# Optimization experiments

Measured on AMD Instinct MI355X. Metric: run time of the kernel, lower is better.

The kernel has to match this reference:

```python
import jax, jax.numpy as jnp
import numpy as np

NUM_HEADS = 16
PROJECT_DIM = 1024
HEAD_DIM = PROJECT_DIM // NUM_HEADS  # 64; used only for the softmax scale


def setup_inputs() -> dict:
    key = jax.random.key(0)
    k1, k2, k3 = jax.random.split(key, 3)
    B, N, D = 8, 3072, PROJECT_DIM
    inputs = jax.random.normal(k1, (B, N, D), dtype=jnp.float32)
    wqkv = jax.random.normal(k2, (D, 3 * D), dtype=jnp.float32) * (1.0 / np.sqrt(D))
    dense_w = jax.random.normal(k3, (3 * D, D), dtype=jnp.float32) * (1.0 / np.sqrt(3 * D))
    dense_b = jnp.zeros((D,), dtype=jnp.float32)
    return {"inputs": inputs, "wqkv": wqkv, "dense_w": dense_w, "dense_b": dense_b}


def reference(inputs, wqkv, dense_w, dense_b):
    B, N, D = inputs.shape
    H = NUM_HEADS
    # fused QKV projection: [B, N, 3D]
    qkv = jnp.einsum('bnd,de->bne', inputs, wqkv)
    # separate heads: [B, H, N, 3*head_dim]
    qkv = qkv.reshape(B, N, H, (3 * D) // H).transpose(0, 2, 1, 3)
    # NOTE: faithful to source — split along TOKEN axis (axis=2) into 3 chunks
    q, k, v = jnp.split(qkv, 3, axis=2)  # each [B, H, N//3, 3*head_dim]
    scale = 1.0 / jnp.sqrt(jnp.float32(HEAD_DIM))
    logits = jnp.einsum('bhqc,bhkc->bhqk', q, k) * scale  # [B, H, N//3, N//3]
    attn = jax.nn.softmax(logits, axis=-1)
    out = jnp.einsum('bhqk,bhkc->bhqc', attn, v)  # [B, H, N//3, 3*head_dim]
    # recombine heads -> [B, N//3, 3D]
    out = out.transpose(0, 2, 1, 3).reshape(B, N // 3, 3 * D)
    # output projection -> [B, N//3, D]
    return jnp.einsum('bnc,cd->bnd', out, dense_w) + dense_b
```

## Files before the change

### kernel.cpp

```cpp
#include <hip/hip_runtime.h>
#include <hip/hip_bf16.h>

typedef unsigned short u16;
using f32x4  = __attribute__((ext_vector_type(4))) float;
using bf16x8 = __attribute__((ext_vector_type(8))) short;

typedef __attribute__((address_space(1))) const void global_cvoid;
typedef __attribute__((address_space(3))) void lds_void;

__device__ __forceinline__ void async16(const u16* g, u16* l) {
    __builtin_amdgcn_global_load_lds((global_cvoid*)g, (lds_void*)l, 16, 0, 0);
}

__device__ __forceinline__ u16 f2bf(float f) {
    union { float f; unsigned u; } cv; cv.f = f;
    unsigned r = cv.u + 0x7fff + ((cv.u >> 16) & 1);
    return (u16)(r >> 16);
}

__device__ __forceinline__ u16 f2bf_rz(float f) {
    union { float f; unsigned u; } cv; cv.f = f;
    return (u16)(cv.u >> 16);
}

__device__ __forceinline__ float dppmax16(float x) {
    union { float f; int i; } c, o;
    c.f = x;
    o.i = __builtin_amdgcn_update_dpp(0, c.i, 0xB1,  0xF, 0xF, true); c.f = fmaxf(c.f, o.f);
    o.i = __builtin_amdgcn_update_dpp(0, c.i, 0x4E,  0xF, 0xF, true); c.f = fmaxf(c.f, o.f);
    o.i = __builtin_amdgcn_update_dpp(0, c.i, 0x141, 0xF, 0xF, true); c.f = fmaxf(c.f, o.f);
    o.i = __builtin_amdgcn_update_dpp(0, c.i, 0x140, 0xF, 0xF, true); c.f = fmaxf(c.f, o.f);
    return c.f;
}

__global__ __launch_bounds__(256) void cast_kernel(const float* __restrict__ src,
                                                   u16* __restrict__ dst, int n4) {
    int i = blockIdx.x * blockDim.x + threadIdx.x;
    int st = gridDim.x * blockDim.x;
    for (; i < n4; i += st) {
        float4 v = ((const float4*)src)[i];
        ushort4 o;
        o.x = f2bf(v.x); o.y = f2bf(v.y); o.z = f2bf(v.z); o.w = f2bf(v.w);
        ((ushort4*)dst)[i] = o;
    }
}

__global__ __launch_bounds__(256) void wtrans_kernel(const float* __restrict__ src,
                                                     u16* __restrict__ dst, int R, int C) {
    __shared__ float tile[64][68];
    int ct = blockIdx.x, rt = blockIdx.y;
    int t = threadIdx.x;
    int r = t >> 2;
    const float* s = src + (size_t)(rt * 64 + r) * C + ct * 64;
#pragma unroll
    for (int jj = 0; jj < 4; ++jj) {
        int c4 = (t & 3) + jj * 4;
        float4 v = *(const float4*)(s + c4 * 4);
        *(float4*)&tile[r][c4 * 4] = v;
    }
    __syncthreads();
    int od = t >> 2;
    u16* d = dst + (size_t)(ct * 64 + od) * R + rt * 64;
#pragma unroll
    for (int jj = 0; jj < 4; ++jj) {
        int c4 = (t & 3) + jj * 4;
        ushort4 v;
        v.x = f2bf(tile[c4 * 4 + 0][od]);
        v.y = f2bf(tile[c4 * 4 + 1][od]);
        v.z = f2bf(tile[c4 * 4 + 2][od]);
        v.w = f2bf(tile[c4 * 4 + 3][od]);
        *(ushort4*)(d + c4 * 4) = v;
    }
}

template<bool OUT_F32>
__global__ __launch_bounds__(256, 2)
void gemm_bt_kernel(const u16* __restrict__ A, const u16* __restrict__ BT,
                    void* __restrict__ Cout, const float* __restrict__ bias,
                    u16* __restrict__ VTout,
                    int M, int N, int K) {
    __shared__ u16 lA[128 * 64];
    __shared__ u16 lB[128 * 64];
    const int t = threadIdx.x;
    const int w = t >> 6, lane = t & 63;
    const int nbx = N >> 7;
    const int nwg = gridDim.x;
    int bid = blockIdx.x;
    int cpx = nwg >> 3;
    int swz = (bid & 7) * cpx + (bid >> 3);
    const int bx = swz % nbx;
    const int by = swz / nbx;
    const size_t m0 = (size_t)by * 128, n0 = (size_t)bx * 128;

    const int lr = lane >> 3;
    const int lc = (lane & 7) * 8;
    const int wr = (w >> 1) * 64, wc = (w & 1) * 64;

    f32x4 acc[4][4] = {};

    for (int kk = 0; kk < K; kk += 64) {
        __syncthreads();
#pragma unroll
        for (int i = 0; i < 4; ++i) {
            int rr = (w * 4 + i) * 8 + lr;
            async16(A  + (m0 + rr) * (size_t)K + kk + lc, &lA[(w * 4 + i) * 512]);
            async16(BT + (n0 + rr) * (size_t)K + kk + lc, &lB[(w * 4 + i) * 512]);
        }
        __syncthreads();
#pragma unroll
        for (int ks = 0; ks < 2; ++ks) {
            bf16x8 af[4], bfv[4];
#pragma unroll
            for (int m = 0; m < 4; ++m)
                af[m] = *(const bf16x8*)&lA[(wr + m * 16 + (lane & 15)) * 64 + ks * 32 + (lane >> 4) * 8];
#pragma unroll
            for (int n = 0; n < 4; ++n)
                bfv[n] = *(const bf16x8*)&lB[(wc + n * 16 + (lane & 15)) * 64 + ks * 32 + (lane >> 4) * 8];
#pragma unroll
            for (int m = 0; m < 4; ++m)
#pragma unroll
                for (int n = 0; n < 4; ++n)
                    acc[m][n] = __builtin_amdgcn_mfma_f32_16x16x32_bf16(af[m], bfv[n], acc[m][n], 0, 0, 0);
        }
    }

    const int r0 = (lane >> 4) * 4;
    const int cl = lane & 15;
    if constexpr (OUT_F32) {
        float* C = (float*)Cout;
#pragma unroll
        for (int m = 0; m < 4; ++m) {
            size_t row = m0 + wr + m * 16 + r0;
#pragma unroll
            for (int n = 0; n < 4; ++n) {
                size_t col = n0 + wc + n * 16 + cl;
                float bv = bias[col];
#pragma unroll
                for (int r = 0; r < 4; ++r)
                    C[(row + r) * (size_t)N + col] = acc[m][n][r] + bv;
            }
        }
    } else {
        u16* C = (u16*)Cout;
#pragma unroll
        for (int m = 0; m < 4; ++m) {
            size_t row = m0 + wr + m * 16 + r0;
#pragma unroll
            for (int n = 0; n < 4; ++n) {
                size_t col = n0 + wc + n * 16 + cl;
#pragma unroll
                for (int r = 0; r < 4; ++r)
                    C[(row + r) * (size_t)N + col] = f2bf(acc[m][n][r]);
            }
        }
    }
}

__global__ __launch_bounds__(512, 2)
void gemm256_kernel(const u16* __restrict__ A, const u16* __restrict__ BT,
                    u16* __restrict__ Cout, u16* __restrict__ VTout,
                    int M, int N, int K) {
    __shared__ u16 lds[65536];
    u16* lA = lds;
    u16* lB = lds + 32768;

    const int t = threadIdx.x, w = t >> 6, l = t & 63;
    const int g = l >> 4, ql = l & 15;
    const int wm = w >> 2, wn = w & 3;
    const int nbx = N >> 8;
    int bid = blockIdx.x;
    int cpx = gridDim.x >> 3;
    int swz = (bid & 7) * cpx + (bid >> 3);
    const int bx = swz % nbx, by = swz / nbx;
    const size_t m0 = (size_t)by * 256, n0 = (size_t)bx * 256;

    const u16* Ag = A  + m0 * (size_t)K;
    const u16* Bg = BT + n0 * (size_t)K;

    unsigned soff[2];
#pragma unroll
    for (int i = 0; i < 2; ++i) {
        int ch = i * 512 + t;
        int r = ch >> 2, c = ch & 3;
        soff[i] = (unsigned)(r * K + (c ^ ((r >> 1) & 3)) * 8);
    }

#define STAGE_PAIR(kh2, i) do {                                                    \
    int sl_ = (kh2) & 3;                                                           \
    async16(Ag + soff[i] + (unsigned)(kh2) * 32u, lA + sl_ * 8192 + ((i) * 512 + w * 64) * 8); \
    async16(Bg + soff[i] + (unsigned)(kh2) * 32u, lB + sl_ * 8192 + ((i) * 512 + w * 64) * 8); \
    } while (0)
#define STAGE_FULL(kh2) do { STAGE_PAIR(kh2, 0); STAGE_PAIR(kh2, 1); } while (0)

    STAGE_FULL(0); STAGE_FULL(1);

    f32x4 acc[8][4] = {};
    const int cswz = (g ^ ((ql >> 1) & 3)) * 8;
    const int arow = wm * 128 + ql;
    const int brow = wn * 64 + ql;

    const int KH = K >> 5;
#pragma unroll 1
    for (int kh = 0; kh < KH; ++kh) {
        if (kh < KH - 1) asm volatile("s_waitcnt vmcnt(4)" ::: "memory");
        else             asm volatile("s_waitcnt vmcnt(0)" ::: "memory");
        __builtin_amdgcn_s_barrier();
        const u16* sA = lA + (kh & 3) * 8192;
        const u16* sB = lB + (kh & 3) * 8192;

        bf16x8 fb[4], fa[4];
#pragma unroll
        for (int n = 0; n < 4; ++n)
            fb[n] = *(const bf16x8*)&sB[(brow + n * 16) * 32 + cswz];
#pragma unroll
        for (int m = 0; m < 4; ++m)
            fa[m] = *(const bf16x8*)&sA[(arow + m * 16) * 32 + cswz];
        if (kh + 2 < KH) STAGE_PAIR(kh + 2, 0);
        __builtin_amdgcn_s_barrier();
        __builtin_amdgcn_s_setprio(1);
#pragma unroll
        for (int m = 0; m < 4; ++m)
#pragma unroll
            for (int n = 0; n < 4; ++n)
                acc[m][n] = __builtin_amdgcn_mfma_f32_16x16x32_bf16(fa[m], fb[n], acc[m][n], 0, 0, 0);
        __builtin_amdgcn_s_setprio(0);

#pragma unroll
        for (int m = 0; m < 4; ++m)
            fa[m] = *(const bf16x8*)&sA[(arow + (m + 4) * 16) * 32 + cswz];
        if (kh + 2 < KH) STAGE_PAIR(kh + 2, 1);
        __builtin_amdgcn_s_barrier();
        __builtin_amdgcn_s_setprio(1);
#pragma unroll
        for (int m = 0; m < 4; ++m)
#pragma unroll
            for (int n = 0; n < 4; ++n)
                acc[m + 4][n] = __builtin_amdgcn_mfma_f32_16x16x32_bf16(fa[m], fb[n], acc[m + 4][n], 0, 0, 0);
        __builtin_amdgcn_s_setprio(0);
    }

    const int r0 = g * 4;
    int tok0 = (int)(m0 % 3072);
    if (tok0 >= 2048) {
        int b = (int)(m0 / 3072);
#pragma unroll
        for (int m = 0; m < 8; ++m) {
            int tok = tok0 - 2048 + wm * 128 + m * 16 + r0;
#pragma unroll
            for (int n = 0; n < 4; ++n) {
                int col = (int)n0 + wn * 64 + n * 16 + ql;
                int h = col / 192, ch = col % 192;
                ushort4 v;
                v.x = f2bf(acc[m][n][0]);
                v.y = f2bf(acc[m][n][1]);
                v.z = f2bf(acc[m][n][2]);
                v.w = f2bf(acc[m][n][3]);
                *(ushort4*)(VTout + ((size_t)(b * 16 + h) * 192 + ch) * 1024 + tok) = v;
            }
        }
    } else {
        float qs = (tok0 < 1024) ? 0.1803368801111f : 1.0f;
#pragma unroll
        for (int m = 0; m < 8; ++m) {
            size_t row = m0 + wm * 128 + m * 16 + r0;
#pragma unroll
            for (int n = 0; n < 4; ++n) {
                size_t col = n0 + wn * 64 + n * 16 + ql;
#pragma unroll
                for (int r = 0; r < 4; ++r)
                    Cout[(row + r) * (size_t)N + col] = f2bf(acc[m][n][r] * qs);
            }
        }
    }
#undef STAGE_PAIR
#undef STAGE_FULL
}

__global__ __launch_bounds__(256, 2)
void attn_kernel(const u16* __restrict__ QKV, const u16* __restrict__ VT,
                 u16* __restrict__ comb) {
    __shared__ u16 lds[40960];
    u16* lK = lds;
    u16* lV = lds + 18432;
    u16* lP = lds + 36864;

    const int t = threadIdx.x, w = t >> 6, lane = t & 63;
    const int g = lane >> 4, ql = lane & 15;
    const int bid = blockIdx.x;
    const int gid = (bid & 7) * 128 + (bid >> 3);
    const int bh = gid >> 3, qt = gid & 7;
    const int b = bh >> 4, h = bh & 15;

    const u16* Qg  = QKV + ((size_t)(b * 3072 + qt * 128 + w * 32)) * 3072 + h * 192;
    const u16* Kg  = QKV + ((size_t)(b * 3072 + 1024)) * 3072 + h * 192;
    const u16* VTg = VT + (size_t)bh * 192 * 1024;

    unsigned koff[3], voff[3];
#pragma unroll
    for (int i = 0; i < 3; ++i) {
        int ch = i * 256 + t;
        int kr = ch / 24, kc = ch % 24;
        koff[i] = kr * 3072 + (kc ^ (kr & 7)) * 8;
        int vr = ch >> 2, vc = ch & 3;
        voff[i] = vr * 1024 + (vc ^ ((vr >> 1) & 3)) * 8;
    }

#define STAGE_KV(kt) do {                                                         \
    int sl_ = (kt) % 3;                                                           \
    _Pragma("unroll")                                                             \
    for (int i = 0; i < 3; ++i) {                                                 \
        async16(Kg + koff[i] + (unsigned)(kt) * 98304u, lK + sl_ * 6144 + (i * 256 + w * 64) * 8); \
        async16(VTg + voff[i] + (unsigned)(kt) * 32u,   lV + sl_ * 6144 + (i * 256 + w * 64) * 8); \
    } } while (0)

    STAGE_KV(0);
    STAGE_KV(1);

    bf16x8 aq[2][6];
#pragma unroll
    for (int rg = 0; rg < 2; ++rg)
#pragma unroll
        for (int cs = 0; cs < 6; ++cs)
            aq[rg][cs] = *(const bf16x8*)(Qg + (size_t)(rg * 16 + ql) * 3072
                                             + cs * 32 + g * 8);

    bf16x8 vone;
#pragma unroll
    for (int j = 0; j < 8; ++j) vone[j] = (short)0x3F80;

    f32x4 acc_o[2][12] = {};
    f32x4 acc_l[2] = {};
    float m2[2] = {-1e30f, -1e30f};
    u16* lPw = &lP[w * 1024];
    const int pswz = (ql >> 2) & 3;

#pragma unroll 1
    for (int it = 0; it < 32; ++it) {
        if (it != 31) asm volatile("s_waitcnt vmcnt(6)" ::: "memory");
        else          asm volatile("s_waitcnt vmcnt(0)" ::: "memory");
        __builtin_amdgcn_s_barrier();
        if (it < 30) STAGE_KV(it + 2);

        const u16* sK = lK + (it % 3) * 6144;
        const u16* sV = lV + (it % 3) * 6144;

        f32x4 s[2][2] = {};
        __builtin_amdgcn_s_setprio(1);
#pragma unroll
        for (int kf = 0; kf < 2; ++kf) {
            const int krow = kf * 16 + ql;
#pragma unroll
            for (int cs = 0; cs < 6; ++cs) {
                bf16x8 bk = *(const bf16x8*)&sK[krow * 192 + ((cs * 4 + g) ^ (krow & 7)) * 8];
                s[0][kf] = __builtin_amdgcn_mfma_f32_16x16x32_bf16(aq[0][cs], bk, s[0][kf], 0, 0, 0);
                s[1][kf] = __builtin_amdgcn_mfma_f32_16x16x32_bf16(aq[1][cs], bk, s[1][kf], 0, 0, 0);
            }
        }
        __builtin_amdgcn_s_setprio(0);

#pragma unroll
        for (int rg = 0; rg < 2; ++rg) {
            float m = s[rg][0][0];
#pragma unroll
            for (int kf = 0; kf < 2; ++kf)
#pragma unroll
                for (int r = 0; r < 4; ++r) m = fmaxf(m, s[rg][kf][r]);
            float mx = dppmax16(m);
            bool need = mx > m2[rg] + 8.f;
            if (__any((int)need)) {
                float mn = fmaxf(m2[rg], mx);
                float fac = exp2f(m2[rg] - mn);
                m2[rg] = mn;
                acc_l[rg] *= fac;
#pragma unroll
                for (int df = 0; df < 12; ++df) acc_o[rg][df] *= fac;
            }
#pragma unroll
            for (int r = 0; r < 4; ++r) {
                int q = rg * 16 + g * 4 + r;
#pragma unroll
                for (int kf = 0; kf < 2; ++kf) {
                    float p = exp2f(s[rg][kf][r] - m2[rg]);
                    lPw[q * 32 + ((kf * 16 + ql) ^ (g << 3))] = f2bf_rz(p);
                }
            }
        }

        __builtin_amdgcn_s_setprio(1);
        {
            bf16x8 pa0 = *(const bf16x8*)&lPw[ql * 32 + ((g ^ pswz) << 3)];
            bf16x8 pa1 = *(const bf16x8*)&lPw[(16 + ql) * 32 + ((g ^ pswz) << 3)];
            acc_l[0] = __builtin_amdgcn_mfma_f32_16x16x32_bf16(pa0, vone, acc_l[0], 0, 0, 0);
            acc_l[1] = __builtin_amdgcn_mfma_f32_16x16x32_bf16(pa1, vone, acc_l[1], 0, 0, 0);
#pragma unroll
            for (int df = 0; df < 12; ++df) {
                const int vrow = df * 16 + ql;
                bf16x8 bv = *(const bf16x8*)&sV[vrow * 32 + ((g ^ ((vrow >> 1) & 3)) << 3)];
                acc_o[0][df] = __builtin_amdgcn_mfma_f32_16x16x32_bf16(pa0, bv, acc_o[0][df], 0, 0, 0);
                acc_o[1][df] = __builtin_amdgcn_mfma_f32_16x16x32_bf16(pa1, bv, acc_o[1][df], 0, 0, 0);
            }
        }
        __builtin_amdgcn_s_setprio(0);
    }

    u16* dst = comb + ((size_t)(b * 1024 + qt * 128 + w * 32)) * 3072 + h * 192;
#pragma unroll
    for (int rg = 0; rg < 2; ++rg)
#pragma unroll
        for (int r = 0; r < 4; ++r) {
            int q = rg * 16 + g * 4 + r;
            float invl = 1.0f / acc_l[rg][r];
#pragma unroll
            for (int df = 0; df < 12; ++df)
                dst[(size_t)q * 3072 + df * 16 + ql] = f2bf(acc_o[rg][df][r] * invl);
        }
#undef STAGE_KV
}

extern "C" void kernel_launch(void* const* d_in, const int* in_sizes, int n_in,
                              void* d_out, int out_size, void* d_ws, size_t ws_size,
                              hipStream_t stream) {
    const float* X  = (const float*)d_in[0];
    const float* W1 = (const float*)d_in[1];
    const float* W2 = (const float*)d_in[2];
    const float* Bb = (const float*)d_in[3];

    char* ws = (char*)d_ws;
    u16* Xb   = (u16*)(ws);
    u16* W1bT = (u16*)(ws + 50331648);
    u16* W2bT = (u16*)(ws + 56623104);
    u16* QKVb = (u16*)(ws + 62914560);
    u16* VT   = (u16*)(ws + 213909504);
    u16* comb = Xb;

    cast_kernel<<<2048, 256, 0, stream>>>(X, Xb, (8 * 3072 * 1024) / 4);
    wtrans_kernel<<<dim3(3072 / 64, 1024 / 64), 256, 0, stream>>>(W1, W1bT, 1024, 3072);
    wtrans_kernel<<<dim3(1024 / 64, 3072 / 64), 256, 0, stream>>>(W2, W2bT, 3072, 1024);
    gemm256_kernel<<<(24576 / 256) * (3072 / 256), 512, 0, stream>>>(
        Xb, W1bT, QKVb, VT, 24576, 3072, 1024);
    attn_kernel<<<1024, 256, 0, stream>>>(QKVb, VT, comb);
    gemm_bt_kernel<true><<<(8192 / 128) * (1024 / 128), 256, 0, stream>>>(
        comb, W2bT, d_out, Bb, nullptr, 8192, 1024, 3072);
}
```

Measured before the change: 395.7 us.

## Switch QKV GEMM to 64-wide K tiles with double-buffered LDS staging

Restructures the QKV projection GEMM main loop from 32-wide K slices in a 4-slot ring (prefetch distance 2) to 64-wide K tiles in two ping-pong buffers with an 8-way XOR swizzle. Each iteration now covers two K sub-steps and issues the next tile's async loads between sub-steps, halving the number of outer iterations and top-of-loop waits. The cost is a full vmcnt(0) wait each iteration and only one tile of prefetch lead, so load latency may be less well hidden.

```diff
diff --git a/kernel.cpp b/kernel.cpp
--- a/kernel.cpp
+++ b/kernel.cpp
@@ -177,66 +177,73 @@
     const u16* Ag = A  + m0 * (size_t)K;
     const u16* Bg = BT + n0 * (size_t)K;
 
-    unsigned soff[2];
-#pragma unroll
-    for (int i = 0; i < 2; ++i) {
+    unsigned soff[4];
+#pragma unroll
+    for (int i = 0; i < 4; ++i) {
         int ch = i * 512 + t;
-        int r = ch >> 2, c = ch & 3;
-        soff[i] = (unsigned)(r * K + (c ^ ((r >> 1) & 3)) * 8);
-    }
-
-#define STAGE_PAIR(kh2, i) do {                                                    \
-    int sl_ = (kh2) & 3;                                                           \
-    async16(Ag + soff[i] + (unsigned)(kh2) * 32u, lA + sl_ * 8192 + ((i) * 512 + w * 64) * 8); \
-    async16(Bg + soff[i] + (unsigned)(kh2) * 32u, lB + sl_ * 8192 + ((i) * 512 + w * 64) * 8); \
+        int r = ch >> 3, c = ch & 7;
+        soff[i] = (unsigned)(r * K + (c ^ (r & 7)) * 8);
+    }
+
+#define STAGE_PAIR(kt1, i) do {                                                    \
+    int bo_ = ((kt1) & 1) * 16384;                                                 \
+    async16(Ag + soff[i] + (unsigned)(kt1) * 64u, lA + bo_ + ((i) * 512 + w * 64) * 8); \
+    async16(Bg + soff[i] + (unsigned)(kt1) * 64u, lB + bo_ + ((i) * 512 + w * 64) * 8); \
     } while (0)
-#define STAGE_FULL(kh2) do { STAGE_PAIR(kh2, 0); STAGE_PAIR(kh2, 1); } while (0)
-
-    STAGE_FULL(0); STAGE_FULL(1);
+
+    STAGE_PAIR(0, 0); STAGE_PAIR(0, 1); STAGE_PAIR(0, 2); STAGE_PAIR(0, 3);
 
     f32x4 acc[8][4] = {};
-    const int cswz = (g ^ ((ql >> 1) & 3)) * 8;
     const int arow = wm * 128 + ql;
     const int brow = wn * 64 + ql;
 
-    const int KH = K >> 5;
+    const int KT = K >> 6;
 #pragma unroll 1
-    for (int kh = 0; kh < KH; ++kh) {
-        if (kh < KH - 1) asm volatile("s_waitcnt vmcnt(4)" ::: "memory");
-        else             asm volatile("s_waitcnt vmcnt(0)" ::: "memory");
+    for (int kt = 0; kt < KT; ++kt) {
+        asm volatile("s_waitcnt vmcnt(0)" ::: "memory");
         __builtin_amdgcn_s_barrier();
-        const u16* sA = lA + (kh & 3) * 8192;
-        const u16* sB = lB + (kh & 3) * 8192;
-
-        bf16x8 fb[4], fa[4];
-#pragma unroll
-        for (int n = 0; n < 4; ++n)
-            fb[n] = *(const bf16x8*)&sB[(brow + n * 16) * 32 + cswz];
-#pragma unroll
-        for (int m = 0; m < 4; ++m)
-            fa[m] = *(const bf16x8*)&sA[(arow + m * 16) * 32 + cswz];
-        if (kh + 2 < KH) STAGE_PAIR(kh + 2, 0);
-        __builtin_amdgcn_s_barrier();
-        __builtin_amdgcn_s_setprio(1);
-#pragma unroll
-        for (int m = 0; m < 4; ++m)
-#pragma unroll
-            for (int n = 0; n < 4; ++n)
-                acc[m][n] = __builtin_amdgcn_mfma_f32_16x16x32_bf16(fa[m], fb[n], acc[m][n], 0, 0, 0);
-        __builtin_amdgcn_s_setprio(0);
-
-#pragma unroll
-        for (int m = 0; m < 4; ++m)
-            fa[m] = *(const bf16x8*)&sA[(arow + (m + 4) * 16) * 32 + cswz];
-        if (kh + 2 < KH) STAGE_PAIR(kh + 2, 1);
-        __builtin_amdgcn_s_barrier();
-        __builtin_amdgcn_s_setprio(1);
-#pragma unroll
-        for (int m = 0; m < 4; ++m)
-#pragma unroll
-            for (int n = 0; n < 4; ++n)
-                acc[m + 4][n] = __builtin_amdgcn_mfma_f32_16x16x32_bf16(fa[m], fb[n], acc[m + 4][n], 0, 0, 0);
-        __builtin_amdgcn_s_setprio(0);
+        const u16* sA = lA + (kt & 1) * 16384;
+        const u16* sB = lB + (kt & 1) * 16384;
+        const bool st = (kt + 1 < KT);
+
+        bf16x8 fa[4], fb[4];
+#pragma unroll
+        for (int ks = 0; ks < 2; ++ks) {
+#pragma unroll
+            for (int m = 0; m < 4; ++m) {
+                int rr = arow + m * 16;
+                fa[m] = *(const bf16x8*)&sA[rr * 64 + ((ks * 4 + g) ^ (rr & 7)) * 8];
+            }
+#pragma unroll
+            for (int n = 0; n < 4; ++n) {
+                int rr = brow + n * 16;
+                fb[n] = *(const bf16x8*)&sB[rr * 64 + ((ks * 4 + g) ^ (rr & 7)) * 8];
+            }
+            if (st) STAGE_PAIR(kt + 1, ks * 2);
+            __builtin_amdgcn_s_barrier();
+            __builtin_amdgcn_s_setprio(1);
+#pragma unroll
+            for (int m = 0; m < 4; ++m)
+#pragma unroll
+                for (int n = 0; n < 4; ++n)
+                    acc[m][n] = __builtin_amdgcn_mfma_f32_16x16x32_bf16(fa[m], fb[n], acc[m][n], 0, 0, 0);
+            __builtin_amdgcn_s_setprio(0);
+
+#pragma unroll
+            for (int m = 0; m < 4; ++m) {
+                int rr = arow + (m + 4) * 16;
+                fa[m] = *(const bf16x8*)&sA[rr * 64 + ((ks * 4 + g) ^ (rr & 7)) * 8];
+            }
+            if (st) STAGE_PAIR(kt + 1, ks * 2 + 1);
+            __builtin_amdgcn_s_barrier();
+            __builtin_amdgcn_s_setprio(1);
+#pragma unroll
+            for (int m = 0; m < 4; ++m)
+#pragma unroll
+                for (int n = 0; n < 4; ++n)
+                    acc[m + 4][n] = __builtin_amdgcn_mfma_f32_16x16x32_bf16(fa[m], fb[n], acc[m + 4][n], 0, 0, 0);
+            __builtin_amdgcn_s_setprio(0);
+        }
     }
 
     const int r0 = g * 4;
@@ -273,7 +280,6 @@
         }
     }
 #undef STAGE_PAIR
-#undef STAGE_FULL
 }
 
 __global__ __launch_bounds__(256, 2)
```

After: 387.9 us. 2.0% less time.
